# Optimization experiments

Measured on AMD Instinct MI355X. Metric: run time of the kernel, lower is better.

Reference implementation:

```python
import jax, jax.numpy as jnp
import numpy as np

B = 1024      # batch
H = 512       # n_hidden
F = 32        # lstm_features
CIN = 4       # input channels
K = 30        # conv kernel
STRIDE = 6
L = 924       # input length -> T = (924-30)//6+1 = 150
KD = 40       # deconv kernel
NSTEPS = 10   # lstm_future_out
DN = ('NCH', 'OIH', 'NCH')


def setup_inputs() -> dict:
    key = jax.random.key(0)
    ks = jax.random.split(key, 14)
    s = 0.05
    rn = lambda k, shape: jax.random.normal(k, shape, jnp.float32) * s
    return dict(
        x=jax.random.normal(ks[0], (B, CIN, L), jnp.float32),
        conv_w=rn(ks[1], (F, CIN, K)), conv_b=rn(ks[2], (F,)),
        Wih0=rn(ks[3], (4 * H, F)), Whh0=rn(ks[4], (4 * H, H)),
        bih0=rn(ks[5], (4 * H,)), bhh0=rn(ks[6], (4 * H,)),
        Wih1=rn(ks[7], (4 * H, H)), Whh1=rn(ks[8], (4 * H, H)),
        bih1=rn(ks[9], (4 * H,)), bhh1=rn(ks[10], (4 * H,)),
        dec_w=rn(ks[11], (F, H)), dec_b=rn(ks[12], (F,)),
        deconv_w=rn(ks[13], (F, 1, KD)),
    )


def _cell(x, h, c, Wih, Whh, b):
    # PyTorch LSTM gate order: i, f, g, o
    g = x @ Wih.T + h @ Whh.T + b
    i, f, gg, o = jnp.split(g, 4, axis=-1)
    c = jax.nn.sigmoid(f) * c + jax.nn.sigmoid(i) * jnp.tanh(gg)
    h = jax.nn.sigmoid(o) * jnp.tanh(c)
    return h, c


def _lstm_layer(seq, Wih, Whh, b):
    # seq: [T, B, in] -> ys: [T, B, H], final (h, c)
    n = seq.shape[1]
    h0 = jnp.zeros((n, H), seq.dtype)
    c0 = jnp.zeros((n, H), seq.dtype)
    def step(carry, x):
        h, c = _cell(x, carry[0], carry[1], Wih, Whh, b)
        return (h, c), h
    (hT, cT), ys = jax.lax.scan(step, (h0, c0), seq)
    return ys, hT, cT


def _forward(x, conv_w, conv_b, Wih0, Whh0, bih0, bhh0,
             Wih1, Whh1, bih1, bhh1, dec_w, dec_b, deconv_w):
    # encoder conv: [B,4,L] -> [B,F,T]
    z = jax.lax.conv_general_dilated(x, conv_w, (STRIDE,), [(0, 0)],
                                     dimension_numbers=DN) + conv_b[None, :, None]
    z = jax.nn.relu(z)
    seq = jnp.transpose(z, (2, 0, 1))  # [T, B, F]
    b0, b1 = bih0 + bhh0, bih1 + bhh1
    s0, h0, c0 = _lstm_layer(seq, Wih0, Whh0, b0)
    s1, h1, c1 = _lstm_layer(s0, Wih1, Whh1, b1)
    out = s1 @ dec_w.T + dec_b                 # [T, B, F]
    y0 = out[-1]                               # output[-2:-1] of encoder -> last decoded step
    def dec_step(carry, _):
        y, ha, ca, hb, cb = carry
        ha, ca = _cell(y, ha, ca, Wih0, Whh0, b0)
        hb, cb = _cell(ha, hb, cb, Wih1, Whh1, b1)
        y = hb @ dec_w.T + dec_b
        return (y, ha, ca, hb, cb), y
    _, fut = jax.lax.scan(dec_step, (y0, h0, c0, h1, c1), None, length=NSTEPS)
    fut = jnp.transpose(fut, (1, 2, 0))        # [B, F, 10]
    # ConvTranspose1d (stride=1, pad=0, no bias) == cross-correlation with
    # spatially flipped, channel-swapped kernel on input padded by KD-1.
    kt = jnp.transpose(jnp.flip(deconv_w, -1), (1, 0, 2))  # [1, F, KD]
    return jax.lax.conv_general_dilated(fut, kt, (1,), [(KD - 1, KD - 1)],
                                        dimension_numbers=DN)  # [B, 1, 49]


def reference(x, conv_w, conv_b, Wih0, Whh0, bih0, bhh0,
              Wih1, Whh1, bih1, bhh1, dec_w, dec_b, deconv_w):
    return _forward(x, conv_w, conv_b, Wih0, Whh0, bih0, bhh0,
                    Wih1, Whh1, bih1, bhh1, dec_w, dec_b, deconv_w)
```

## Files before the change

kernel.cpp:

```cpp
#include <hip/hip_runtime.h>
#include <hip/hip_bf16.h>

typedef __hip_bfloat16 bf16;
typedef __attribute__((ext_vector_type(8))) short short8;
typedef __attribute__((ext_vector_type(4))) float float4v;

#define B_    1024
#define H_    512
#define G4H   2048
#define F_    32
#define CIN_  4
#define K_    30
#define STRIDE_ 6
#define L_    924
#define T_    150
#define KD_   40
#define NSTEPS_ 10
#define BH    (B_ * H_)
#define STRF  16

__device__ __forceinline__ float sigmoidf_(float x) { return 1.f / (1.f + __expf(-x)); }
__device__ __forceinline__ float tanhf_(float x)    { return 1.f - 2.f / (__expf(2.f * x) + 1.f); }
__device__ __forceinline__ float b2f_(short s) {
    return __uint_as_float(((unsigned)(unsigned short)s) << 16);
}
__device__ __forceinline__ unsigned short f2bu_(float v) {
    union { __hip_bfloat16 b; unsigned short u; } cv;
    cv.b = __float2bfloat16(v);
    return cv.u;
}
__device__ __forceinline__ void stwt_(bf16* p, float v) {
    __hip_atomic_store((unsigned short*)p, f2bu_(v), __ATOMIC_RELAXED, __HIP_MEMORY_SCOPE_AGENT);
}

__global__ __launch_bounds__(256) void cvt_kernel(const float* __restrict__ src,
                                                  bf16* __restrict__ dst, int n) {
    int i = blockIdx.x * 256 + threadIdx.x;
    if (i < n) dst[i] = __float2bfloat16(src[i]);
}

__global__ void bias_kernel(const float* __restrict__ bih0, const float* __restrict__ bhh0,
                            const float* __restrict__ bih1, const float* __restrict__ bhh1,
                            float* __restrict__ b0, float* __restrict__ b1) {
    int i = blockIdx.x * 256 + threadIdx.x;
    if (i < G4H)      b0[i] = bih0[i] + bhh0[i];
    else if (i < 2*G4H) { int j = i - G4H; b1[j] = bih1[j] + bhh1[j]; }
}

__global__ __launch_bounds__(256) void conv_kernel(
    const float* __restrict__ x, const float* __restrict__ w,
    const float* __restrict__ cb, bf16* __restrict__ seq)
{
    __shared__ float w_lds[CIN_ * K_ * F_];
    __shared__ float x_lds[CIN_ * L_];
    int tid = threadIdx.x;
    int b = blockIdx.x;
    for (int i = tid; i < CIN_ * K_ * F_; i += 256) {
        int f = i & 31, r = i >> 5;
        w_lds[r * 32 + f] = w[f * (CIN_ * K_) + r];
    }
    const float* xb = x + (size_t)b * (CIN_ * L_);
    for (int i = tid; i < CIN_ * L_; i += 256)
        x_lds[i] = xb[i];
    __syncthreads();
    int f = tid & 31, tt = tid >> 5;
    float cbf = cb[f];
    for (int t0 = 0; t0 < T_; t0 += 8) {
        int t = t0 + tt;
        if (t < T_) {
            float acc = cbf;
            #pragma unroll
            for (int c = 0; c < CIN_; ++c) {
                const float* xr = x_lds + c * L_ + t * STRIDE_;
                const float* wr = w_lds + c * K_ * 32 + f;
                #pragma unroll
                for (int k = 0; k < K_; ++k)
                    acc += xr[k] * wr[k * 32];
            }
            acc = fmaxf(acc, 0.f);
            seq[(size_t)t * (B_ * F_) + b * F_ + f] = __float2bfloat16(acc);
        }
    }
}

__device__ __forceinline__ void wait2(const int* fa, int ta, const int* fb, int tb) {
    const int t = threadIdx.x;
    if (t < 64) {
        const int* p = nullptr; int tgt = 0;
        if (t < 32) { if (fa) { p = fa + t * STRF;        tgt = ta; } }
        else        { if (fb) { p = fb + (t - 32) * STRF; tgt = tb; } }
        for (;;) {
            int v = p ? __hip_atomic_load(p, __ATOMIC_RELAXED, __HIP_MEMORY_SCOPE_AGENT)
                      : 0x7fffffff;
            if (__all(v >= tgt)) break;
            __builtin_amdgcn_s_sleep(2);
        }
    }
    __syncthreads();
    __builtin_amdgcn_fence(__ATOMIC_ACQUIRE, "agent");
}

__device__ __forceinline__ void signal1(int* f, int val) {
    __syncthreads();
    if (threadIdx.x == 0) {
        __builtin_amdgcn_s_waitcnt(0);
        __hip_atomic_store(f, val, __ATOMIC_RELAXED, __HIP_MEMORY_SCOPE_AGENT);
    }
}

template<int P1KS, int XSTR>
__device__ __forceinline__ void layer_step(
    const bf16* __restrict__ X, const bf16* __restrict__ Hprev,
    const short8* __restrict__ WldsH, const short8* __restrict__ WldsI,
    float bi, float bff, float bg, float bo,
    float (&creg)[16], bf16* __restrict__ Hout,
    int m0, int j0, int wid, int lane)
{
    const int row16 = lane & 15;
    const int quad  = lane >> 4;
    const int mrow  = m0 + wid * 64 + row16;

    float4v acc[4][4];
    #pragma unroll
    for (int ms = 0; ms < 4; ++ms)
        #pragma unroll
        for (int g = 0; g < 4; ++g)
            acc[ms][g] = (float4v){0.f, 0.f, 0.f, 0.f};

    for (int ks = 0; ks < P1KS; ++ks) {
        short8 av[4];
        #pragma unroll
        for (int ms = 0; ms < 4; ++ms)
            av[ms] = *(const short8*)(X + (size_t)(mrow + ms * 16) * XSTR
                                      + ks * 32 + quad * 8);
        #pragma unroll
        for (int g = 0; g < 4; ++g) {
            short8 bfr = WldsI[(ks * 4 + g) * 64 + lane];
            #pragma unroll
            for (int ms = 0; ms < 4; ++ms)
                acc[ms][g] = __builtin_amdgcn_mfma_f32_16x16x32_bf16(av[ms], bfr, acc[ms][g], 0, 0, 0);
        }
    }

    for (int ks = 0; ks < 16; ++ks) {
        short8 av[4];
        #pragma unroll
        for (int ms = 0; ms < 4; ++ms)
            av[ms] = *(const short8*)(Hprev + (size_t)(mrow + ms * 16) * H_
                                      + ks * 32 + quad * 8);
        #pragma unroll
        for (int g = 0; g < 4; ++g) {
            short8 bfr = WldsH[(ks * 4 + g) * 64 + lane];
            #pragma unroll
            for (int ms = 0; ms < 4; ++ms)
                acc[ms][g] = __builtin_amdgcn_mfma_f32_16x16x32_bf16(av[ms], bfr, acc[ms][g], 0, 0, 0);
        }
    }

    float hval[16];
    #pragma unroll
    for (int ms = 0; ms < 4; ++ms) {
        #pragma unroll
        for (int r = 0; r < 4; ++r) {
            float ig = sigmoidf_(acc[ms][0][r] + bi);
            float fg = sigmoidf_(acc[ms][1][r] + bff);
            float gg = tanhf_(acc[ms][2][r] + bg);
            float og = sigmoidf_(acc[ms][3][r] + bo);
            float cn = fg * creg[ms * 4 + r] + ig * gg;
            creg[ms * 4 + r] = cn;
            hval[ms * 4 + r] = og * tanhf_(cn);
        }
    }

    unsigned wA[16];
    #pragma unroll
    for (int i = 0; i < 16; ++i) {
        float o = __shfl_xor(hval[i], 1);
        float lo = (lane & 1) ? o : hval[i];
        float hi = (lane & 1) ? hval[i] : o;
        wA[i] = (unsigned)f2bu_(lo) | ((unsigned)f2bu_(hi) << 16);
    }
    unsigned long long q[16];
    #pragma unroll
    for (int i = 0; i < 16; ++i) {
        unsigned o2 = __shfl_xor(wA[i], 2);
        q[i] = (lane & 2) ? (((unsigned long long)wA[i] << 32) | o2)
                          : (((unsigned long long)o2 << 32) | wA[i]);
    }
    const int cchunk = j0 + (row16 & ~3);
    #pragma unroll
    for (int i = 0; i < 16; ++i) {
        if ((i >> 2) == (lane & 3)) {
            int ms = i >> 2, r = i & 3;
            size_t off = (size_t)(m0 + wid * 64 + ms * 16 + quad * 4 + r) * H_ + cchunk;
            __hip_atomic_store((unsigned long long*)(Hout + off), q[i],
                               __ATOMIC_RELAXED, __HIP_MEMORY_SCOPE_AGENT);
        }
    }
}

struct PP {
    const bf16 *seq, *Wih0, *Whh0, *Wih1, *Whh1, *dwb;
    const float *b0, *b1, *dec_b;
    float *fut;
    bf16 *h0, *h1, *y;
    int *flags;
};

__global__ __launch_bounds__(256, 1) void lstm_persist(PP P) {
    __shared__ short8 WldsH[4096];
    __shared__ short8 WldsI[4096];

    const int bid   = blockIdx.x;
    const int gsw   = bid & 7;
    const bool isL0 = (gsw < 4);
    const int mg    = gsw & 3;
    const int jj    = bid >> 3;
    const int lb    = mg * 32 + jj;
    const int j0    = jj * 16;
    const int m0    = mg * 256;
    const int tid   = threadIdx.x;
    const int wid   = tid >> 6;
    const int lane  = tid & 63;

    {
        const bf16* Whh = isL0 ? P.Whh0 : P.Whh1;
        for (int i = 0; i < 16; ++i) {
            int s = tid + i * 256;
            int frag = s >> 6, ln = s & 63;
            int ks = frag >> 2, g = frag & 3;
            WldsH[s] = *(const short8*)(Whh + (size_t)(g * H_ + j0 + (ln & 15)) * H_
                                        + ks * 32 + (ln >> 4) * 8);
        }
        if (isL0) {
            int frag = tid >> 6, ln = tid & 63;
            int g = frag & 3;
            WldsI[tid] = *(const short8*)(P.Wih0 + (size_t)(g * H_ + j0 + (ln & 15)) * F_
                                          + (ln >> 4) * 8);
        } else {
            for (int i = 0; i < 16; ++i) {
                int s = tid + i * 256;
                int frag = s >> 6, ln = s & 63;
                int ks = frag >> 2, g = frag & 3;
                WldsI[s] = *(const short8*)(P.Wih1 + (size_t)(g * H_ + j0 + (ln & 15)) * H_
                                            + ks * 32 + (ln >> 4) * 8);
            }
        }
        __syncthreads();
    }

    const float* bias = isL0 ? P.b0 : P.b1;
    const int jb  = j0 + (lane & 15);
    const float bi  = bias[jb];
    const float bff = bias[H_ + jb];
    const float bg  = bias[2 * H_ + jb];
    const float bo  = bias[3 * H_ + jb];

    float creg[16];
    #pragma unroll
    for (int i = 0; i < 16; ++i) creg[i] = 0.f;

    int* f0 = P.flags;
    int* f1 = P.flags + 128 * STRF;
    int* fy = P.flags + 256 * STRF;
    const int* f0g = f0 + mg * 32 * STRF;
    const int* f1g = f1 + mg * 32 * STRF;
    const int* fyg = fy + mg * 32 * STRF;

    if (isL0) {
        for (int t = 0; t < T_; ++t) {
            wait2(f0g, t, f1g, t - 2);
            layer_step<1, 32>(P.seq + (size_t)t * B_ * F_,
                              P.h0 + (size_t)((t + 2) % 3) * BH, WldsH, WldsI,
                              bi, bff, bg, bo,
                              creg, P.h0 + (size_t)(t % 3) * BH, m0, j0, wid, lane);
            signal1(f0 + lb * STRF, t + 1);
        }
        for (int s = 0; s <= NSTEPS_; ++s) {
            wait2(f1g, T_ + s, (s >= 1) ? f0g : nullptr, T_ + s);
            {
                int id = lb * 256 + tid;
                int br = id >> 5, f = id & 31;
                const short8* hv = (const short8*)(P.h1 + (size_t)((T_ - 1 + s) % 3) * BH
                                                   + (size_t)br * H_);
                const short8* wv = (const short8*)(P.dwb + (size_t)f * H_);
                float acc = P.dec_b[f];
                for (int i = 0; i < H_ / 8; ++i) {
                    short8 h8 = hv[i], w8 = wv[i];
                    #pragma unroll
                    for (int k = 0; k < 8; ++k)
                        acc += b2f_(h8[k]) * b2f_(w8[k]);
                }
                stwt_(P.y + id, acc);
                if (s >= 1)
                    P.fut[(size_t)br * (F_ * NSTEPS_) + f * NSTEPS_ + (s - 1)] = acc;
            }
            signal1(fy + lb * STRF, s + 1);
            if (s < NSTEPS_) {
                int t = T_ + s;
                wait2(f0g, t, f1g, t - 2);
                wait2(fyg, s + 1, nullptr, 0);
                layer_step<1, 32>(P.y,
                                  P.h0 + (size_t)((t + 2) % 3) * BH, WldsH, WldsI,
                                  bi, bff, bg, bo,
                                  creg, P.h0 + (size_t)(t % 3) * BH, m0, j0, wid, lane);
                signal1(f0 + lb * STRF, t + 1);
            }
        }
    } else {
        for (int t = 0; t < T_ + NSTEPS_; ++t) {
            wait2(f0g, t + 1, f1g, t);
            layer_step<16, 512>(P.h0 + (size_t)(t % 3) * BH,
                                P.h1 + (size_t)((t + 2) % 3) * BH, WldsH, WldsI,
                                bi, bff, bg, bo,
                                creg, P.h1 + (size_t)(t % 3) * BH, m0, j0, wid, lane);
            signal1(f1 + lb * STRF, t + 1);
        }
    }
}

__global__ __launch_bounds__(256) void deconv_kernel(
    const float* __restrict__ fut, const float* __restrict__ dw,
    float* __restrict__ out)
{
    int idx = blockIdx.x * 256 + threadIdx.x;
    if (idx >= B_ * 49) return;
    int b = idx / 49, jj = idx % 49;
    int tlo = jj - (KD_ - 1); if (tlo < 0) tlo = 0;
    int thi = jj; if (thi > NSTEPS_ - 1) thi = NSTEPS_ - 1;
    float acc = 0.f;
    for (int f = 0; f < F_; ++f) {
        const float* fr = fut + (size_t)b * (F_ * NSTEPS_) + f * NSTEPS_;
        const float* wr = dw + f * KD_;
        for (int t = tlo; t <= thi; ++t)
            acc += fr[t] * wr[jj - t];
    }
    out[idx] = acc;
}

extern "C" void kernel_launch(void* const* d_in, const int* in_sizes, int n_in,
                              void* d_out, int out_size, void* d_ws, size_t ws_size,
                              hipStream_t stream) {
    const float* x       = (const float*)d_in[0];
    const float* conv_w  = (const float*)d_in[1];
    const float* conv_b  = (const float*)d_in[2];
    const float* Wih0f   = (const float*)d_in[3];
    const float* Whh0f   = (const float*)d_in[4];
    const float* bih0    = (const float*)d_in[5];
    const float* bhh0    = (const float*)d_in[6];
    const float* Wih1f   = (const float*)d_in[7];
    const float* Whh1f   = (const float*)d_in[8];
    const float* bih1    = (const float*)d_in[9];
    const float* bhh1    = (const float*)d_in[10];
    const float* dec_wf  = (const float*)d_in[11];
    const float* dec_b   = (const float*)d_in[12];
    const float* deconvw = (const float*)d_in[13];
    float* out = (float*)d_out;

    char* ws = (char*)d_ws;
    size_t off = 0;
    auto alloc = [&](size_t bytes) { char* p = ws + off; off = (off + bytes + 255) & ~(size_t)255; return p; };
    bf16*  seq   = (bf16*) alloc((size_t)T_ * B_ * F_ * 2);
    float* b0v   = (float*)alloc(G4H * 4);
    float* b1v   = (float*)alloc(G4H * 4);
    bf16*  h0    = (bf16*) alloc((size_t)3 * BH * 2);
    bf16*  h1    = (bf16*) alloc((size_t)3 * BH * 2);
    bf16*  y     = (bf16*) alloc((size_t)B_ * F_ * 2);
    float* fut   = (float*)alloc((size_t)B_ * F_ * NSTEPS_ * 4);
    bf16*  Wih0b = (bf16*) alloc((size_t)G4H * F_ * 2);
    bf16*  Whh0b = (bf16*) alloc((size_t)G4H * H_ * 2);
    bf16*  Wih1b = (bf16*) alloc((size_t)G4H * H_ * 2);
    bf16*  Whh1b = (bf16*) alloc((size_t)G4H * H_ * 2);
    bf16*  dec_wb= (bf16*) alloc((size_t)F_ * H_ * 2);
    int*   flags = (int*)  alloc(3 * 128 * STRF * 4);

    hipMemsetAsync(h0, 0, (size_t)3 * BH * 2, stream);
    hipMemsetAsync(h1, 0, (size_t)3 * BH * 2, stream);
    hipMemsetAsync(flags, 0, 3 * 128 * STRF * 4, stream);

    cvt_kernel<<<(G4H * F_ + 255) / 256, 256, 0, stream>>>(Wih0f, Wih0b, G4H * F_);
    cvt_kernel<<<(G4H * H_ + 255) / 256, 256, 0, stream>>>(Whh0f, Whh0b, G4H * H_);
    cvt_kernel<<<(G4H * H_ + 255) / 256, 256, 0, stream>>>(Wih1f, Wih1b, G4H * H_);
    cvt_kernel<<<(G4H * H_ + 255) / 256, 256, 0, stream>>>(Whh1f, Whh1b, G4H * H_);
    cvt_kernel<<<(F_ * H_ + 255) / 256, 256, 0, stream>>>(dec_wf, dec_wb, F_ * H_);

    bias_kernel<<<16, 256, 0, stream>>>(bih0, bhh0, bih1, bhh1, b0v, b1v);
    conv_kernel<<<B_, 256, 0, stream>>>(x, conv_w, conv_b, seq);

    PP P;
    P.seq = seq; P.Wih0 = Wih0b; P.Whh0 = Whh0b; P.Wih1 = Wih1b; P.Whh1 = Whh1b;
    P.dwb = dec_wb; P.b0 = b0v; P.b1 = b1v; P.dec_b = dec_b;
    P.fut = fut; P.h0 = h0; P.h1 = h1; P.y = y;
    P.flags = flags;

    void* args[] = { &P };
    hipError_t err = hipLaunchCooperativeKernel((const void*)lstm_persist,
                                                dim3(256), dim3(256), args, 0, stream);
    if (err != hipSuccess) {
        lstm_persist<<<256, 256, 0, stream>>>(P);
    }

    deconv_kernel<<<196, 256, 0, stream>>>(fut, deconvw, out);
}
```

Before: 5.013 ms.

## Repartition persistent LSTM blocks per XCD with wider hidden tiles and global Wih1

Reassigns the 256 persistent blocks so each XCD owns a 128-row batch slice, with 16 blocks per layer each covering 32 hidden units. Flag waits then only poll 16 peers that sit on the same XCD, which keeps the inter-block sync traffic local to that die's L2. Layer-1 input weights Wih1 are no longer staged in LDS and are read from global memory each step, to fit the doubled Whh tile in LDS. The risk is extra global or L2 weight traffic per timestep for layer 1, traded against faster synchronization.

Measured after the change: 6.477 ms. 1.29x slower.

```diff
diff --git a/kernel.cpp b/kernel.cpp
--- a/kernel.cpp
+++ b/kernel.cpp
@@ -17,6 +17,7 @@
 #define KD_   40
 #define NSTEPS_ 10
 #define BH    (B_ * H_)
+#define LROWS 128
 #define STRF  16
 
 __device__ __forceinline__ float sigmoidf_(float x) { return 1.f / (1.f + __expf(-x)); }
@@ -87,8 +88,8 @@
     const int t = threadIdx.x;
     if (t < 64) {
         const int* p = nullptr; int tgt = 0;
-        if (t < 32) { if (fa) { p = fa + t * STRF;        tgt = ta; } }
-        else        { if (fb) { p = fb + (t - 32) * STRF; tgt = tb; } }
+        if (t < 16)               { if (fa) { p = fa + t * STRF;        tgt = ta; } }
+        else if (t < 32)          { if (fb) { p = fb + (t - 16) * STRF; tgt = tb; } }
         for (;;) {
             int v = p ? __hip_atomic_load(p, __ATOMIC_RELAXED, __HIP_MEMORY_SCOPE_AGENT)
                       : 0x7fffffff;
@@ -108,67 +109,71 @@
     }
 }
 
-template<int P1KS, int XSTR>
+template<int P1KS, int XSTR, bool WG>
 __device__ __forceinline__ void layer_step(
     const bf16* __restrict__ X, const bf16* __restrict__ Hprev,
     const short8* __restrict__ WldsH, const short8* __restrict__ WldsI,
-    float bi, float bff, float bg, float bo,
-    float (&creg)[16], bf16* __restrict__ Hout,
+    const bf16* __restrict__ WihG,
+    const float (&bv)[4][2], float (&creg)[16], bf16* __restrict__ Hout,
     int m0, int j0, int wid, int lane)
 {
     const int row16 = lane & 15;
     const int quad  = lane >> 4;
-    const int mrow  = m0 + wid * 64 + row16;
-
-    float4v acc[4][4];
-    #pragma unroll
-    for (int ms = 0; ms < 4; ++ms)
+    const int mrow  = m0 + wid * 32 + row16;
+
+    float4v acc[2][8];
+    #pragma unroll
+    for (int mt = 0; mt < 2; ++mt)
         #pragma unroll
-        for (int g = 0; g < 4; ++g)
-            acc[ms][g] = (float4v){0.f, 0.f, 0.f, 0.f};
-
-    for (int ks = 0; ks < P1KS; ++ks) {
-        short8 av[4];
+        for (int c = 0; c < 8; ++c)
+            acc[mt][c] = (float4v){0.f, 0.f, 0.f, 0.f};
+
+    const bf16* wgb = WG ? (WihG + (size_t)(j0 + row16) * H_ + quad * 8) : nullptr;
+
+    for (int kg = 0; kg < P1KS; ++kg) {
+        short8 av0 = *(const short8*)(X + (size_t)mrow * XSTR + kg * 32 + quad * 8);
+        short8 av1 = *(const short8*)(X + (size_t)(mrow + 16) * XSTR + kg * 32 + quad * 8);
         #pragma unroll
-        for (int ms = 0; ms < 4; ++ms)
-            av[ms] = *(const short8*)(X + (size_t)(mrow + ms * 16) * XSTR
-                                      + ks * 32 + quad * 8);
+        for (int ctg = 0; ctg < 8; ++ctg) {
+            short8 bfr;
+            if constexpr (WG) {
+                const size_t off = ((size_t)(ctg >> 1) * 512 + (ctg & 1) * 16) * H_;
+                bfr = *(const short8*)(wgb + off + kg * 32);
+            } else {
+                bfr = WldsI[(kg * 8 + ctg) * 64 + lane];
+            }
+            acc[0][ctg] = __builtin_amdgcn_mfma_f32_16x16x32_bf16(av0, bfr, acc[0][ctg], 0, 0, 0);
+            acc[1][ctg] = __builtin_amdgcn_mfma_f32_16x16x32_bf16(av1, bfr, acc[1][ctg], 0, 0, 0);
+        }
+    }
+
+    for (int kg = 0; kg < 16; ++kg) {
+        short8 av0 = *(const short8*)(Hprev + (size_t)mrow * H_ + kg * 32 + quad * 8);
+        short8 av1 = *(const short8*)(Hprev + (size_t)(mrow + 16) * H_ + kg * 32 + quad * 8);
         #pragma unroll
-        for (int g = 0; g < 4; ++g) {
-            short8 bfr = WldsI[(ks * 4 + g) * 64 + lane];
+        for (int ctg = 0; ctg < 8; ++ctg) {
+            short8 bfr = WldsH[(kg * 8 + ctg) * 64 + lane];
+            acc[0][ctg] = __builtin_amdgcn_mfma_f32_16x16x32_bf16(av0, bfr, acc[0][ctg], 0, 0, 0);
+            acc[1][ctg] = __builtin_amdgcn_mfma_f32_16x16x32_bf16(av1, bfr, acc[1][ctg], 0, 0, 0);
+        }
+    }
+
+    float hval[16];
+    #pragma unroll
+    for (int mt = 0; mt < 2; ++mt) {
+        #pragma unroll
+        for (int ct = 0; ct < 2; ++ct) {
             #pragma unroll
-            for (int ms = 0; ms < 4; ++ms)
-                acc[ms][g] = __builtin_amdgcn_mfma_f32_16x16x32_bf16(av[ms], bfr, acc[ms][g], 0, 0, 0);
-        }
-    }
-
-    for (int ks = 0; ks < 16; ++ks) {
-        short8 av[4];
-        #pragma unroll
-        for (int ms = 0; ms < 4; ++ms)
-            av[ms] = *(const short8*)(Hprev + (size_t)(mrow + ms * 16) * H_
-                                      + ks * 32 + quad * 8);
-        #pragma unroll
-        for (int g = 0; g < 4; ++g) {
-            short8 bfr = WldsH[(ks * 4 + g) * 64 + lane];
-            #pragma unroll
-            for (int ms = 0; ms < 4; ++ms)
-                acc[ms][g] = __builtin_amdgcn_mfma_f32_16x16x32_bf16(av[ms], bfr, acc[ms][g], 0, 0, 0);
-        }
-    }
-
-    float hval[16];
-    #pragma unroll
-    for (int ms = 0; ms < 4; ++ms) {
-        #pragma unroll
-        for (int r = 0; r < 4; ++r) {
-            float ig = sigmoidf_(acc[ms][0][r] + bi);
-            float fg = sigmoidf_(acc[ms][1][r] + bff);
-            float gg = tanhf_(acc[ms][2][r] + bg);
-            float og = sigmoidf_(acc[ms][3][r] + bo);
-            float cn = fg * creg[ms * 4 + r] + ig * gg;
-            creg[ms * 4 + r] = cn;
-            hval[ms * 4 + r] = og * tanhf_(cn);
+            for (int rr = 0; rr < 4; ++rr) {
+                int idx = (mt * 2 + ct) * 4 + rr;
+                float ig = sigmoidf_(acc[mt][0 * 2 + ct][rr] + bv[0][ct]);
+                float fg = sigmoidf_(acc[mt][1 * 2 + ct][rr] + bv[1][ct]);
+                float gg = tanhf_(acc[mt][2 * 2 + ct][rr] + bv[2][ct]);
+                float og = sigmoidf_(acc[mt][3 * 2 + ct][rr] + bv[3][ct]);
+                float cn = fg * creg[idx] + ig * gg;
+                creg[idx] = cn;
+                hval[idx] = og * tanhf_(cn);
+            }
         }
     }
 
@@ -187,13 +192,13 @@
         q[i] = (lane & 2) ? (((unsigned long long)wA[i] << 32) | o2)
                           : (((unsigned long long)o2 << 32) | wA[i]);
     }
-    const int cchunk = j0 + (row16 & ~3);
     #pragma unroll
     for (int i = 0; i < 16; ++i) {
         if ((i >> 2) == (lane & 3)) {
-            int ms = i >> 2, r = i & 3;
-            size_t off = (size_t)(m0 + wid * 64 + ms * 16 + quad * 4 + r) * H_ + cchunk;
-            __hip_atomic_store((unsigned long long*)(Hout + off), q[i],
+            int mt = i >> 3, ct = (i >> 2) & 1, rr = i & 3;
+            int brow = m0 + wid * 32 + mt * 16 + quad * 4 + rr;
+            int cch  = j0 + ct * 16 + (row16 & ~3);
+            __hip_atomic_store((unsigned long long*)(Hout + (size_t)brow * H_ + cch), q[i],
                                __ATOMIC_RELAXED, __HIP_MEMORY_SCOPE_AGENT);
         }
     }
@@ -208,53 +213,50 @@
 };
 
 __global__ __launch_bounds__(256, 1) void lstm_persist(PP P) {
-    __shared__ short8 WldsH[4096];
-    __shared__ short8 WldsI[4096];
+    __shared__ short8 WldsH[16 * 8 * 64];
+    __shared__ short8 WldsI[8 * 64];
 
     const int bid   = blockIdx.x;
-    const int gsw   = bid & 7;
-    const bool isL0 = (gsw < 4);
-    const int mg    = gsw & 3;
-    const int jj    = bid >> 3;
-    const int lb    = mg * 32 + jj;
-    const int j0    = jj * 16;
-    const int m0    = mg * 256;
+    const int xcd   = bid & 7;
+    const int role  = bid >> 3;
+    const bool isL0 = (role < 16);
+    const int r     = isL0 ? role : role - 16;
+    const int j0    = r * 32;
+    const int m0    = xcd * LROWS;
     const int tid   = threadIdx.x;
     const int wid   = tid >> 6;
     const int lane  = tid & 63;
+    const int row16 = lane & 15;
 
     {
         const bf16* Whh = isL0 ? P.Whh0 : P.Whh1;
-        for (int i = 0; i < 16; ++i) {
+        for (int i = 0; i < 32; ++i) {
             int s = tid + i * 256;
             int frag = s >> 6, ln = s & 63;
-            int ks = frag >> 2, g = frag & 3;
-            WldsH[s] = *(const short8*)(Whh + (size_t)(g * H_ + j0 + (ln & 15)) * H_
-                                        + ks * 32 + (ln >> 4) * 8);
+            int kg = frag >> 3, ctg = frag & 7;
+            int g = ctg >> 1, ct = ctg & 1;
+            WldsH[s] = *(const short8*)(Whh + (size_t)(g * 512 + j0 + ct * 16 + (ln & 15)) * H_
+                                        + kg * 32 + (ln >> 4) * 8);
         }
         if (isL0) {
-            int frag = tid >> 6, ln = tid & 63;
-            int g = frag & 3;
-            WldsI[tid] = *(const short8*)(P.Wih0 + (size_t)(g * H_ + j0 + (ln & 15)) * F_
-                                          + (ln >> 4) * 8);
-        } else {
-            for (int i = 0; i < 16; ++i) {
+            for (int i = 0; i < 2; ++i) {
                 int s = tid + i * 256;
-                int frag = s >> 6, ln = s & 63;
-                int ks = frag >> 2, g = frag & 3;
-                WldsI[s] = *(const short8*)(P.Wih1 + (size_t)(g * H_ + j0 + (ln & 15)) * H_
-                                            + ks * 32 + (ln >> 4) * 8);
+                int ctg = s >> 6, ln = s & 63;
+                int g = ctg >> 1, ct = ctg & 1;
+                WldsI[s] = *(const short8*)(P.Wih0 + (size_t)(g * 512 + j0 + ct * 16 + (ln & 15)) * F_
+                                            + (ln >> 4) * 8);
             }
         }
         __syncthreads();
     }
 
     const float* bias = isL0 ? P.b0 : P.b1;
-    const int jb  = j0 + (lane & 15);
-    const float bi  = bias[jb];
-    const float bff = bias[H_ + jb];
-    const float bg  = bias[2 * H_ + jb];
-    const float bo  = bias[3 * H_ + jb];
+    float bv[4][2];
+    #pragma unroll
+    for (int g = 0; g < 4; ++g)
+        #pragma unroll
+        for (int ct = 0; ct < 2; ++ct)
+            bv[g][ct] = bias[g * 512 + j0 + ct * 16 + row16];
 
     float creg[16];
     #pragma unroll
@@ -263,26 +265,26 @@
     int* f0 = P.flags;
     int* f1 = P.flags + 128 * STRF;
     int* fy = P.flags + 256 * STRF;
-    const int* f0g = f0 + mg * 32 * STRF;
-    const int* f1g = f1 + mg * 32 * STRF;
-    const int* fyg = fy + mg * 32 * STRF;
+    int* f0x = f0 + xcd * 16 * STRF;
+    int* f1x = f1 + xcd * 16 * STRF;
+    int* fyx = fy + xcd * 16 * STRF;
 
     if (isL0) {
         for (int t = 0; t < T_; ++t) {
-            wait2(f0g, t, f1g, t - 2);
-            layer_step<1, 32>(P.seq + (size_t)t * B_ * F_,
-                              P.h0 + (size_t)((t + 2) % 3) * BH, WldsH, WldsI,
-                              bi, bff, bg, bo,
-                              creg, P.h0 + (size_t)(t % 3) * BH, m0, j0, wid, lane);
-            signal1(f0 + lb * STRF, t + 1);
+            wait2(f0x, t, f1x, t - 2);
+            layer_step<1, 32, false>(P.seq + (size_t)t * B_ * F_,
+                              P.h0 + (size_t)((t + 2) % 3) * BH, WldsH, WldsI, nullptr,
+                              bv, creg, P.h0 + (size_t)(t % 3) * BH, m0, j0, wid, lane);
+            signal1(f0x + r * STRF, t + 1);
         }
         for (int s = 0; s <= NSTEPS_; ++s) {
-            wait2(f1g, T_ + s, (s >= 1) ? f0g : nullptr, T_ + s);
+            wait2(f1x, T_ + s, (s >= 1) ? f0x : nullptr, T_ + s);
             {
-                int id = lb * 256 + tid;
-                int br = id >> 5, f = id & 31;
+                int id = r * 256 + tid;
+                int lr = id >> 5, f = id & 31;
+                int grow = m0 + lr;
                 const short8* hv = (const short8*)(P.h1 + (size_t)((T_ - 1 + s) % 3) * BH
-                                                   + (size_t)br * H_);
+                                                   + (size_t)grow * H_);
                 const short8* wv = (const short8*)(P.dwb + (size_t)f * H_);
                 float acc = P.dec_b[f];
                 for (int i = 0; i < H_ / 8; ++i) {
@@ -291,30 +293,28 @@
                     for (int k = 0; k < 8; ++k)
                         acc += b2f_(h8[k]) * b2f_(w8[k]);
                 }
-                stwt_(P.y + id, acc);
+                stwt_(P.y + (size_t)grow * F_ + f, acc);
                 if (s >= 1)
-                    P.fut[(size_t)br * (F_ * NSTEPS_) + f * NSTEPS_ + (s - 1)] = acc;
-            }
-            signal1(fy + lb * STRF, s + 1);
+                    P.fut[(size_t)grow * (F_ * NSTEPS_) + f * NSTEPS_ + (s - 1)] = acc;
+            }
+            signal1(fyx + r * STRF, s + 1);
             if (s < NSTEPS_) {
                 int t = T_ + s;
-                wait2(f0g, t, f1g, t - 2);
-                wait2(fyg, s + 1, nullptr, 0);
-                layer_step<1, 32>(P.y,
-                                  P.h0 + (size_t)((t + 2) % 3) * BH, WldsH, WldsI,
-                                  bi, bff, bg, bo,
-                                  creg, P.h0 + (size_t)(t % 3) * BH, m0, j0, wid, lane);
-                signal1(f0 + lb * STRF, t + 1);
+                wait2(f0x, t, f1x, t - 2);
+                wait2(fyx, s + 1, nullptr, 0);
+                layer_step<1, 32, false>(P.y,
+                                  P.h0 + (size_t)((t + 2) % 3) * BH, WldsH, WldsI, nullptr,
+                                  bv, creg, P.h0 + (size_t)(t % 3) * BH, m0, j0, wid, lane);
+                signal1(f0x + r * STRF, t + 1);
             }
         }
     } else {
         for (int t = 0; t < T_ + NSTEPS_; ++t) {
-            wait2(f0g, t + 1, f1g, t);
-            layer_step<16, 512>(P.h0 + (size_t)(t % 3) * BH,
-                                P.h1 + (size_t)((t + 2) % 3) * BH, WldsH, WldsI,
-                                bi, bff, bg, bo,
-                                creg, P.h1 + (size_t)(t % 3) * BH, m0, j0, wid, lane);
-            signal1(f1 + lb * STRF, t + 1);
+            wait2(f0x, t + 1, f1x, t);
+            layer_step<16, 512, true>(P.h0 + (size_t)(t % 3) * BH,
+                                P.h1 + (size_t)((t + 2) % 3) * BH, WldsH, nullptr, P.Wih1,
+                                bv, creg, P.h1 + (size_t)(t % 3) * BH, m0, j0, wid, lane);
+            signal1(f1x + r * STRF, t + 1);
         }
     }
 }
```

## Split hidden-state writes into fast local-cache path and deferred write-through copy

Applied to the files above, without the earlier changes.

Each LSTM step now writes its hidden tile with plain (cacheable) stores for consumers that share the same cache, then signals a fast flag, and afterwards issues the agent-scope write-through atomic stores of the same data. A second set of slow flags tells cross-group consumers (layer 1 reading layer 0, the decoder reading h1) when the write-through copy is visible. The intent is to take the costly coherent stores off the critical path of the recurrence. In exchange it adds extra flag traffic and depends on the fast and slow readers being grouped correctly for memory visibility. There is a risk of stale reads if that grouping assumption does not hold.

Result: no change. 4.968 ms (-0.9%).

```diff
diff --git a/kernel.cpp b/kernel.cpp
--- a/kernel.cpp
+++ b/kernel.cpp
@@ -28,9 +28,6 @@
     union { __hip_bfloat16 b; unsigned short u; } cv;
     cv.b = __float2bfloat16(v);
     return cv.u;
-}
-__device__ __forceinline__ void stwt_(bf16* p, float v) {
-    __hip_atomic_store((unsigned short*)p, f2bu_(v), __ATOMIC_RELAXED, __HIP_MEMORY_SCOPE_AGENT);
 }
 
 __global__ __launch_bounds__(256) void cvt_kernel(const float* __restrict__ src,
@@ -108,12 +105,32 @@
     }
 }
 
+__device__ __forceinline__ void signal_slow(int* f, int val) {
+    __syncthreads();
+    if (threadIdx.x == 0) {
+        __builtin_amdgcn_s_waitcnt(0);
+        __hip_atomic_store(f, val, __ATOMIC_RELAXED, __HIP_MEMORY_SCOPE_AGENT);
+    }
+}
+
+__device__ __forceinline__ void wt_stores(bf16* Hwt, const unsigned long long (&qv)[4],
+                                          int m0, int j0, int wid, int lane) {
+    const int row16 = lane & 15, quad = lane >> 4, ms = lane & 3;
+    const int cchunk = j0 + (row16 & ~3);
+    #pragma unroll
+    for (int r = 0; r < 4; ++r) {
+        size_t off = (size_t)(m0 + wid * 64 + ms * 16 + quad * 4 + r) * H_ + cchunk;
+        __hip_atomic_store((unsigned long long*)(Hwt + off), qv[r],
+                           __ATOMIC_RELAXED, __HIP_MEMORY_SCOPE_AGENT);
+    }
+}
+
 template<int P1KS, int XSTR>
 __device__ __forceinline__ void layer_step(
     const bf16* __restrict__ X, const bf16* __restrict__ Hprev,
     const short8* __restrict__ WldsH, const short8* __restrict__ WldsI,
     float bi, float bff, float bg, float bo,
-    float (&creg)[16], bf16* __restrict__ Hout,
+    float (&creg)[16], bf16* __restrict__ Hout, unsigned long long (&qout)[4],
     int m0, int j0, int wid, int lane)
 {
     const int row16 = lane & 15;
@@ -193,8 +210,8 @@
         if ((i >> 2) == (lane & 3)) {
             int ms = i >> 2, r = i & 3;
             size_t off = (size_t)(m0 + wid * 64 + ms * 16 + quad * 4 + r) * H_ + cchunk;
-            __hip_atomic_store((unsigned long long*)(Hout + off), q[i],
-                               __ATOMIC_RELAXED, __HIP_MEMORY_SCOPE_AGENT);
+            *(unsigned long long*)(Hout + off) = q[i];
+            qout[i & 3] = q[i];
         }
     }
 }
@@ -260,24 +277,32 @@
     #pragma unroll
     for (int i = 0; i < 16; ++i) creg[i] = 0.f;
 
-    int* f0 = P.flags;
-    int* f1 = P.flags + 128 * STRF;
-    int* fy = P.flags + 256 * STRF;
-    const int* f0g = f0 + mg * 32 * STRF;
-    const int* f1g = f1 + mg * 32 * STRF;
-    const int* fyg = fy + mg * 32 * STRF;
+    int* f0f = P.flags;
+    int* f1f = P.flags + 128 * STRF;
+    int* fy  = P.flags + 256 * STRF;
+    int* f0s = P.flags + 384 * STRF;
+    int* f1s = P.flags + 512 * STRF;
+    const int* f0fg = f0f + mg * 32 * STRF;
+    const int* f1fg = f1f + mg * 32 * STRF;
+    const int* fyg  = fy  + mg * 32 * STRF;
+    const int* f0sg = f0s + mg * 32 * STRF;
+    const int* f1sg = f1s + mg * 32 * STRF;
 
     if (isL0) {
         for (int t = 0; t < T_; ++t) {
-            wait2(f0g, t, f1g, t - 2);
+            signal_slow(f0s + lb * STRF, t);
+            wait2(f0fg, t, f1fg, t - 2);
+            unsigned long long qv[4];
             layer_step<1, 32>(P.seq + (size_t)t * B_ * F_,
                               P.h0 + (size_t)((t + 2) % 3) * BH, WldsH, WldsI,
                               bi, bff, bg, bo,
-                              creg, P.h0 + (size_t)(t % 3) * BH, m0, j0, wid, lane);
-            signal1(f0 + lb * STRF, t + 1);
+                              creg, P.h0 + (size_t)(t % 3) * BH, qv, m0, j0, wid, lane);
+            signal1(f0f + lb * STRF, t + 1);
+            wt_stores(P.h0 + (size_t)(t % 3) * BH, qv, m0, j0, wid, lane);
         }
         for (int s = 0; s <= NSTEPS_; ++s) {
-            wait2(f1g, T_ + s, (s >= 1) ? f0g : nullptr, T_ + s);
+            signal_slow(f0s + lb * STRF, T_ + s);
+            wait2(f1sg, T_ + s, (s >= 1) ? f0fg : nullptr, T_ + s);
             {
                 int id = lb * 256 + tid;
                 int br = id >> 5, f = id & 31;
@@ -291,31 +316,38 @@
                     for (int k = 0; k < 8; ++k)
                         acc += b2f_(h8[k]) * b2f_(w8[k]);
                 }
-                stwt_(P.y + id, acc);
+                P.y[id] = __float2bfloat16(acc);
                 if (s >= 1)
                     P.fut[(size_t)br * (F_ * NSTEPS_) + f * NSTEPS_ + (s - 1)] = acc;
             }
             signal1(fy + lb * STRF, s + 1);
             if (s < NSTEPS_) {
                 int t = T_ + s;
-                wait2(f0g, t, f1g, t - 2);
+                wait2(f0fg, t, f1fg, t - 2);
                 wait2(fyg, s + 1, nullptr, 0);
+                unsigned long long qv[4];
                 layer_step<1, 32>(P.y,
                                   P.h0 + (size_t)((t + 2) % 3) * BH, WldsH, WldsI,
                                   bi, bff, bg, bo,
-                                  creg, P.h0 + (size_t)(t % 3) * BH, m0, j0, wid, lane);
-                signal1(f0 + lb * STRF, t + 1);
+                                  creg, P.h0 + (size_t)(t % 3) * BH, qv, m0, j0, wid, lane);
+                signal1(f0f + lb * STRF, t + 1);
+                wt_stores(P.h0 + (size_t)(t % 3) * BH, qv, m0, j0, wid, lane);
             }
         }
     } else {
         for (int t = 0; t < T_ + NSTEPS_; ++t) {
-            wait2(f0g, t + 1, f1g, t);
+            signal_slow(f1s + lb * STRF, t);
+            wait2(f0sg, t + 1, f1fg, t);
+            unsigned long long qv[4];
             layer_step<16, 512>(P.h0 + (size_t)(t % 3) * BH,
                                 P.h1 + (size_t)((t + 2) % 3) * BH, WldsH, WldsI,
                                 bi, bff, bg, bo,
-                                creg, P.h1 + (size_t)(t % 3) * BH, m0, j0, wid, lane);
-            signal1(f1 + lb * STRF, t + 1);
-        }
+                                creg, P.h1 + (size_t)(t % 3) * BH, qv, m0, j0, wid, lane);
+            signal1(f1f + lb * STRF, t + 1);
+            if (t >= T_ - 1)
+                wt_stores(P.h1 + (size_t)(t % 3) * BH, qv, m0, j0, wid, lane);
+        }
+        signal_slow(f1s + lb * STRF, T_ + NSTEPS_);
     }
 }
 
@@ -372,11 +404,11 @@
     bf16*  Wih1b = (bf16*) alloc((size_t)G4H * H_ * 2);
     bf16*  Whh1b = (bf16*) alloc((size_t)G4H * H_ * 2);
     bf16*  dec_wb= (bf16*) alloc((size_t)F_ * H_ * 2);
-    int*   flags = (int*)  alloc(3 * 128 * STRF * 4);
+    int*   flags = (int*)  alloc(5 * 128 * STRF * 4);
 
     hipMemsetAsync(h0, 0, (size_t)3 * BH * 2, stream);
     hipMemsetAsync(h1, 0, (size_t)3 * BH * 2, stream);
-    hipMemsetAsync(flags, 0, 3 * 128 * STRF * 4, stream);
+    hipMemsetAsync(flags, 0, 5 * 128 * STRF * 4, stream);
 
     cvt_kernel<<<(G4H * F_ + 255) / 256, 256, 0, stream>>>(Wih0f, Wih0b, G4H * F_);
     cvt_kernel<<<(G4H * H_ + 255) / 256, 256, 0, stream>>>(Whh0f, Whh0b, G4H * H_);
```
